# Kernel tuning notes

Measured on AMD Instinct MI355X. Metric: run time of the kernel, lower is better.

Reference implementation:

```python
import jax, jax.numpy as jnp
import numpy as np

ALPHA = 20.0 / 100.0  # dt / tau
ONE_MINUS_ALPHA = 1.0 - ALPHA


def setup_inputs() -> dict:
    key = jax.random.key(0)
    ks = jax.random.split(key, 7)
    T, B, I, H, O = 512, 256, 256, 1024, 128
    si, sh, so = 1.0 / np.sqrt(I), 1.0 / np.sqrt(H), 1.0 / np.sqrt(H)
    return {
        "x": jax.random.normal(ks[0], (T, B, I), dtype=jnp.float32),
        "Wi": jax.random.normal(ks[1], (H, I), dtype=jnp.float32) * si,
        "bi": jax.random.normal(ks[2], (H,), dtype=jnp.float32) * si,
        "Wh": jax.random.normal(ks[3], (H, H), dtype=jnp.float32) * sh,
        "bh": jax.random.normal(ks[4], (H,), dtype=jnp.float32) * sh,
        "Wo": jax.random.normal(ks[5], (O, H), dtype=jnp.float32) * so,
        "bo": jax.random.normal(ks[6], (O,), dtype=jnp.float32) * so,
    }


def reference(x, Wi, bi, Wh, bh, Wo, bo):
    T, B, I = x.shape
    H = Wh.shape[0]
    # Precompute input projection for all timesteps: [T, B, H]
    inp_proj = jnp.einsum("tbi,hi->tbh", x, Wi) + bi

    def step(carry, u_t):
        state, out = carry
        total = u_t + out @ Wh.T + bh
        state = state * ONE_MINUS_ALPHA + total * ALPHA
        out = jax.nn.relu(state)
        return (state, out), out

    init = (jnp.zeros((B, H), x.dtype), jnp.zeros((B, H), x.dtype))
    (_, _), rnn_activity = jax.lax.scan(step, init, inp_proj)  # [T, B, H]
    out = jnp.einsum("tbh,oh->tbo", rnn_activity, Wo) + bo  # [T, B, O]
    return out, rnn_activity
```

## Files before the change

kernel.cpp:

```cpp
#include <hip/hip_runtime.h>

using f4_t  = __attribute__((ext_vector_type(4))) float;
using bf8_t = __attribute__((ext_vector_type(8))) short;
using u32x4 = __attribute__((ext_vector_type(4))) unsigned int;

#define T_DIM 512
#define B_DIM 256
#define I_DIM 256
#define H_DIM 1024
#define O_DIM 128

#define SWZ(row, byte) ((byte) ^ (((row) & 7) << 4))

#define SMASK 0x8000800080008000ull

__device__ __forceinline__ unsigned short f2bf(float f) {
  unsigned u = __builtin_bit_cast(unsigned, f);
  return (unsigned short)((u + 0x7FFFu + ((u >> 16) & 1u)) >> 16);
}

__device__ __forceinline__ unsigned long long pack4bf(f4_t v) {
  unsigned long long r;
  r  = (unsigned long long)f2bf(v[0]);
  r |= (unsigned long long)f2bf(v[1]) << 16;
  r |= (unsigned long long)f2bf(v[2]) << 32;
  r |= (unsigned long long)f2bf(v[3]) << 48;
  return r;
}

__global__ __launch_bounds__(256, 1) void k_init(
    const float* __restrict__ Wi, const float* __restrict__ Wh,
    const float* __restrict__ Wo, unsigned short* __restrict__ Wi_b,
    unsigned short* __restrict__ Wh_b, unsigned short* __restrict__ Wo_b,
    unsigned short* __restrict__ hbuf1, unsigned* __restrict__ done) {
  int idx = blockIdx.x * 256 + threadIdx.x;
  int stride = gridDim.x * 256;
  for (int i = idx; i < H_DIM * H_DIM; i += stride) Wh_b[i] = f2bf(Wh[i]);
  for (int i = idx; i < H_DIM * I_DIM; i += stride) Wi_b[i] = f2bf(Wi[i]);
  for (int i = idx; i < O_DIM * H_DIM; i += stride) Wo_b[i] = f2bf(Wo[i]);
  for (int i = idx; i < B_DIM * H_DIM; i += stride) hbuf1[i] = 0x8000;
  for (int i = idx; i < 256 * 32; i += stride) done[i] = 0;
}

__global__ __launch_bounds__(256, 2) void k_inproj(
    const float* __restrict__ x, const unsigned short* __restrict__ Wi_b,
    const float* __restrict__ bi, float* __restrict__ act) {
  __shared__ unsigned short As[128 * 128];
  __shared__ unsigned short Bs[128 * 128];
  int blk = blockIdx.x;
  int mb = (blk & 7) * 128 + (blk >> 6);
  int nb = (blk >> 3) & 7;
  int m0 = mb * 128, n0 = nb * 128;
  int tid = threadIdx.x;
  int lane = tid & 63, w = tid >> 6;
  int wm0 = (w & 1) * 64, wn0 = (w >> 1) * 64;
  int lrow = lane & 15, lk = (lane >> 4) * 8;
  f4_t acc[4][4];
#pragma unroll
  for (int a = 0; a < 4; ++a)
#pragma unroll
    for (int b = 0; b < 4; ++b) acc[a][b] = (f4_t){0.f, 0.f, 0.f, 0.f};

  for (int kb = 0; kb < 2; ++kb) {
    if (kb) __syncthreads();
#pragma unroll
    for (int it = 0; it < 16; ++it) {
      int c = it * 256 + tid;
      int row = c >> 5;
      int kc = (c & 31) * 4;
      f4_t v = *(const f4_t*)(x + (size_t)(m0 + row) * I_DIM + kb * 128 + kc);
      *(unsigned long long*)((char*)As + SWZ(row, row * 256 + kc * 2)) = pack4bf(v);
    }
#pragma unroll
    for (int it = 0; it < 8; ++it) {
      int c = it * 256 + tid;
      int row = c >> 4;
      int k16 = c & 15;
      u32x4 v = *(const u32x4*)(Wi_b + (size_t)(n0 + row) * I_DIM + kb * 128 + k16 * 8);
      *(u32x4*)((char*)Bs + SWZ(row, row * 256 + k16 * 16)) = v;
    }
    __syncthreads();
#pragma unroll
    for (int ks = 0; ks < 4; ++ks) {
      bf8_t aF[4], bF[4];
#pragma unroll
      for (int mt = 0; mt < 4; ++mt) {
        int row = wm0 + mt * 16 + lrow;
        aF[mt] = *(const bf8_t*)((char*)As + SWZ(row, row * 256 + (ks * 32 + lk) * 2));
      }
#pragma unroll
      for (int nt = 0; nt < 4; ++nt) {
        int row = wn0 + nt * 16 + lrow;
        bF[nt] = *(const bf8_t*)((char*)Bs + SWZ(row, row * 256 + (ks * 32 + lk) * 2));
      }
#pragma unroll
      for (int mt = 0; mt < 4; ++mt)
#pragma unroll
        for (int nt = 0; nt < 4; ++nt)
          acc[mt][nt] =
              __builtin_amdgcn_mfma_f32_16x16x32_bf16(aF[mt], bF[nt], acc[mt][nt], 0, 0, 0);
    }
  }
#pragma unroll
  for (int nt = 0; nt < 4; ++nt) {
    int col = n0 + wn0 + nt * 16 + lrow;
    float bv = bi[col];
#pragma unroll
    for (int mt = 0; mt < 4; ++mt) {
      int rbase = m0 + wm0 + mt * 16 + (lane >> 4) * 4;
#pragma unroll
      for (int r = 0; r < 4; ++r)
        act[(size_t)(rbase + r) * H_DIM + col] = acc[mt][nt][r] + bv;
    }
  }
}

__global__ __launch_bounds__(256, 1) void k_scan(
    const unsigned short* __restrict__ Wh_b, const float* __restrict__ bh,
    float* __restrict__ act, unsigned short* __restrict__ hbuf0,
    unsigned short* __restrict__ hbuf1, unsigned* __restrict__ done) {
  __shared__ __align__(16) char hT[16 * 2048];
  __shared__ __align__(16) float pbuf[4][16][68];
  int blk = blockIdx.x;
  int g = blk & 15, hs = blk >> 4;
  int b0 = g * 16, h0 = hs * 64;
  int tid = threadIdx.x;
  int lane = tid & 63, w = tid >> 6;
  int lrow = lane & 15, lgq = lane >> 4, lk = lgq * 8;

  bf8_t Bf[4][8];
#pragma unroll
  for (int n = 0; n < 4; ++n)
#pragma unroll
    for (int kc = 0; kc < 8; ++kc)
      Bf[n][kc] = *(const bf8_t*)(Wh_b + (size_t)(h0 + n * 16 + lrow) * H_DIM +
                                  w * 256 + kc * 32 + lk);

  int pr = tid >> 4, pc = (tid & 15) * 4;
  float st[4] = {0.f, 0.f, 0.f, 0.f};
  f4_t bh4 = *(const f4_t*)(bh + h0 + pc);

  unsigned short* hb[2] = {hbuf0, hbuf1};
  unsigned* myslot = done + (g * 16 + hs) * 32;
  const unsigned* pollp = done + (g * 16 + (lane & 15)) * 32;
  bool dopoll = (lane < 16) && (lane != hs);

  int rh = tid >> 7;
  int colb = (tid & 127) * 16;

  f4_t ucur = *(const f4_t*)(act + (size_t)(b0 + pr) * H_DIM + h0 + pc);

  for (int t = 0; t < T_DIM; ++t) {
    int p = t & 1;
    const unsigned short* hprev = hb[p ^ 1];
    unsigned wtag = ((unsigned)(t - 1) >> 1) & 1u;
    unsigned want32 = wtag ? 0x80008000u : 0u;

    if (t > 0 && dopoll) {
      int gd = 0;
      while (__hip_atomic_load(pollp, __ATOMIC_RELAXED, __HIP_MEMORY_SCOPE_AGENT) <
                 (unsigned)t &&
             ++gd < 60000)
        __builtin_amdgcn_s_sleep(1);
    }
    __builtin_amdgcn_sched_barrier(0);

    const char* base = (const char*)(hprev + (size_t)b0 * H_DIM);
    unsigned long long a0 = (unsigned long long)(base + tid * 16);
    u32x4 q0, q1, q2, q3, q4, q5, q6, q7;
    asm volatile(
        "global_load_dwordx4 %[d0], %[a0], off sc0 sc1\n\t"
        "global_load_dwordx4 %[d1], %[a1], off sc0 sc1\n\t"
        "global_load_dwordx4 %[d2], %[a2], off sc0 sc1\n\t"
        "global_load_dwordx4 %[d3], %[a3], off sc0 sc1\n\t"
        "global_load_dwordx4 %[d4], %[a4], off sc0 sc1\n\t"
        "global_load_dwordx4 %[d5], %[a5], off sc0 sc1\n\t"
        "global_load_dwordx4 %[d6], %[a6], off sc0 sc1\n\t"
        "global_load_dwordx4 %[d7], %[a7], off sc0 sc1\n\t"
        "s_waitcnt vmcnt(0)"
        : [d0] "=&v"(q0), [d1] "=&v"(q1), [d2] "=&v"(q2), [d3] "=&v"(q3),
          [d4] "=&v"(q4), [d5] "=&v"(q5), [d6] "=&v"(q6), [d7] "=&v"(q7)
        : [a0] "v"(a0), [a1] "v"(a0 + 4096), [a2] "v"(a0 + 8192),
          [a3] "v"(a0 + 12288), [a4] "v"(a0 + 16384), [a5] "v"(a0 + 20480),
          [a6] "v"(a0 + 24576), [a7] "v"(a0 + 28672)
        : "memory");
    __builtin_amdgcn_sched_barrier(0);

    int tn = (t + 1 < T_DIM) ? t + 1 : t;
    f4_t unext = *(const f4_t*)(act + ((size_t)tn * B_DIM + b0 + pr) * H_DIM + h0 + pc);

#define STALE(qq) \
  ((((qq[0] ^ want32) | (qq[1] ^ want32) | (qq[2] ^ want32) | (qq[3] ^ want32)) & \
    0x80008000u) != 0u)
#define RELOAD(qq, ad)                                                          \
  asm volatile("global_load_dwordx4 %0, %1, off sc0 sc1\n\ts_waitcnt vmcnt(0)"  \
               : "=&v"(qq)                                                      \
               : "v"(ad)                                                        \
               : "memory")
    {
      int vg = 0;
      for (;;) {
        unsigned m = (STALE(q0) ? 1u : 0u) | (STALE(q1) ? 2u : 0u) |
                     (STALE(q2) ? 4u : 0u) | (STALE(q3) ? 8u : 0u) |
                     (STALE(q4) ? 16u : 0u) | (STALE(q5) ? 32u : 0u) |
                     (STALE(q6) ? 64u : 0u) | (STALE(q7) ? 128u : 0u);
        if (m == 0u || ++vg >= 400) break;
        __builtin_amdgcn_s_sleep(1);
        if (m & 1u) RELOAD(q0, a0);
        if (m & 2u) RELOAD(q1, a0 + 4096);
        if (m & 4u) RELOAD(q2, a0 + 8192);
        if (m & 8u) RELOAD(q3, a0 + 12288);
        if (m & 16u) RELOAD(q4, a0 + 16384);
        if (m & 32u) RELOAD(q5, a0 + 20480);
        if (m & 64u) RELOAD(q6, a0 + 24576);
        if (m & 128u) RELOAD(q7, a0 + 28672);
      }
    }
#undef STALE
#undef RELOAD
#pragma unroll
    for (int d = 0; d < 4; ++d) {
      q0[d] &= 0x7fff7fffu; q1[d] &= 0x7fff7fffu; q2[d] &= 0x7fff7fffu;
      q3[d] &= 0x7fff7fffu; q4[d] &= 0x7fff7fffu; q5[d] &= 0x7fff7fffu;
      q6[d] &= 0x7fff7fffu; q7[d] &= 0x7fff7fffu;
    }

#define STAGE(qq, r)                                                            \
  *(u32x4*)(&hT[(2 * (r) + rh) * 2048 + SWZ(2 * (r) + rh, colb)]) = qq
    STAGE(q0, 0); STAGE(q1, 1); STAGE(q2, 2); STAGE(q3, 3);
    STAGE(q4, 4); STAGE(q5, 5); STAGE(q6, 6); STAGE(q7, 7);
#undef STAGE
    asm volatile("s_waitcnt lgkmcnt(0)\ns_barrier" ::: "memory");
    __builtin_amdgcn_sched_barrier(0);

    f4_t acc[4];
#pragma unroll
    for (int n = 0; n < 4; ++n) acc[n] = (f4_t){0.f, 0.f, 0.f, 0.f};
#pragma unroll
    for (int kc = 0; kc < 8; ++kc) {
      int cbyte = w * 512 + kc * 64 + lgq * 16;
      bf8_t Af = *(const bf8_t*)(&hT[lrow * 2048 + SWZ(lrow, cbyte)]);
#pragma unroll
      for (int n = 0; n < 4; ++n)
        acc[n] = __builtin_amdgcn_mfma_f32_16x16x32_bf16(Af, Bf[n][kc], acc[n], 0, 0, 0);
    }

#pragma unroll
    for (int n = 0; n < 4; ++n)
#pragma unroll
      for (int r = 0; r < 4; ++r)
        pbuf[w][lgq * 4 + r][n * 16 + lrow] = acc[n][r];
    asm volatile("s_waitcnt lgkmcnt(0)\ns_barrier" ::: "memory");
    __builtin_amdgcn_sched_barrier(0);

    f4_t s0 = *(const f4_t*)&pbuf[0][pr][pc];
    f4_t s1 = *(const f4_t*)&pbuf[1][pr][pc];
    f4_t s2 = *(const f4_t*)&pbuf[2][pr][pc];
    f4_t s3 = *(const f4_t*)&pbuf[3][pr][pc];
    f4_t tot = s0 + s1 + s2 + s3 + ucur + bh4;
    f4_t hres;
#pragma unroll
    for (int j = 0; j < 4; ++j) {
      st[j] = st[j] * 0.8f + tot[j] * 0.2f;
      hres[j] = fmaxf(st[j], 0.f);
    }

    unsigned long long hp = pack4bf(hres) | (((t >> 1) & 1) ? SMASK : 0ull);
    __hip_atomic_store(
        (unsigned long long*)(hb[p] + (size_t)(b0 + pr) * H_DIM + h0 + pc), hp,
        __ATOMIC_RELAXED, __HIP_MEMORY_SCOPE_AGENT);

    asm volatile("s_barrier" ::: "memory");
    if (tid == 0)
      __hip_atomic_store(myslot, (unsigned)(t + 1), __ATOMIC_RELAXED,
                         __HIP_MEMORY_SCOPE_AGENT);

    *(f4_t*)(act + ((size_t)t * B_DIM + b0 + pr) * H_DIM + h0 + pc) = hres;
    ucur = unext;
  }
}

__global__ __launch_bounds__(256, 2) void k_outproj(
    const float* __restrict__ act, const unsigned short* __restrict__ Wo_b,
    const float* __restrict__ bo, float* __restrict__ out) {
  __shared__ unsigned short As[128 * 64];
  __shared__ unsigned short Bs[128 * 64];
  int m0 = blockIdx.x * 128;
  int tid = threadIdx.x;
  int lane = tid & 63, w = tid >> 6;
  int wm0 = (w & 1) * 64, wn0 = (w >> 1) * 64;
  int lrow = lane & 15, lk = (lane >> 4) * 8;
  f4_t acc[4][4];
#pragma unroll
  for (int a = 0; a < 4; ++a)
#pragma unroll
    for (int b = 0; b < 4; ++b) acc[a][b] = (f4_t){0.f, 0.f, 0.f, 0.f};

  for (int kb = 0; kb < 16; ++kb) {
    if (kb) __syncthreads();
#pragma unroll
    for (int it = 0; it < 8; ++it) {
      int c = it * 256 + tid;
      int row = c >> 4;
      int kc = (c & 15) * 4;
      f4_t v = *(const f4_t*)(act + (size_t)(m0 + row) * H_DIM + kb * 64 + kc);
      *(unsigned long long*)((char*)As + SWZ(row, row * 128 + kc * 2)) = pack4bf(v);
    }
#pragma unroll
    for (int it = 0; it < 4; ++it) {
      int c = it * 256 + tid;
      int row = c >> 3;
      int k16 = c & 7;
      u32x4 v = *(const u32x4*)(Wo_b + (size_t)row * H_DIM + kb * 64 + k16 * 8);
      *(u32x4*)((char*)Bs + SWZ(row, row * 128 + k16 * 16)) = v;
    }
    __syncthreads();
#pragma unroll
    for (int ks = 0; ks < 2; ++ks) {
      bf8_t aF[4], bF[4];
#pragma unroll
      for (int mt = 0; mt < 4; ++mt) {
        int row = wm0 + mt * 16 + lrow;
        aF[mt] = *(const bf8_t*)((char*)As + SWZ(row, row * 128 + (ks * 32 + lk) * 2));
      }
#pragma unroll
      for (int nt = 0; nt < 4; ++nt) {
        int row = wn0 + nt * 16 + lrow;
        bF[nt] = *(const bf8_t*)((char*)Bs + SWZ(row, row * 128 + (ks * 32 + lk) * 2));
      }
#pragma unroll
      for (int mt = 0; mt < 4; ++mt)
#pragma unroll
        for (int nt = 0; nt < 4; ++nt)
          acc[mt][nt] =
              __builtin_amdgcn_mfma_f32_16x16x32_bf16(aF[mt], bF[nt], acc[mt][nt], 0, 0, 0);
    }
  }
#pragma unroll
  for (int nt = 0; nt < 4; ++nt) {
    int col = wn0 + nt * 16 + lrow;
    float bv = bo[col];
#pragma unroll
    for (int mt = 0; mt < 4; ++mt) {
      int rbase = m0 + wm0 + mt * 16 + (lane >> 4) * 4;
#pragma unroll
      for (int r = 0; r < 4; ++r)
        out[(size_t)(rbase + r) * O_DIM + col] = acc[mt][nt][r] + bv;
    }
  }
}

extern "C" void kernel_launch(void* const* d_in, const int* in_sizes, int n_in,
                              void* d_out, int out_size, void* d_ws, size_t ws_size,
                              hipStream_t stream) {
  const float* x  = (const float*)d_in[0];
  const float* Wi = (const float*)d_in[1];
  const float* bi = (const float*)d_in[2];
  const float* Wh = (const float*)d_in[3];
  const float* bh = (const float*)d_in[4];
  const float* Wo = (const float*)d_in[5];
  const float* bo = (const float*)d_in[6];

  float* out = (float*)d_out;
  float* act = out + (size_t)T_DIM * B_DIM * O_DIM;

  char* ws = (char*)d_ws;
  unsigned short* Wh_b  = (unsigned short*)(ws);
  unsigned short* Wi_b  = (unsigned short*)(ws + (2u << 20));
  unsigned short* Wo_b  = (unsigned short*)(ws + (2u << 20) + (512u << 10));
  unsigned short* hbuf0 = (unsigned short*)(ws + (2u << 20) + (768u << 10));
  unsigned short* hbuf1 = (unsigned short*)(ws + (2u << 20) + (1280u << 10));
  unsigned* done        = (unsigned*)(ws + (2u << 20) + (1792u << 10));

  k_init<<<1024, 256, 0, stream>>>(Wi, Wh, Wo, Wi_b, Wh_b, Wo_b, hbuf1, done);
  k_inproj<<<8192, 256, 0, stream>>>(x, Wi_b, bi, act);
  k_scan<<<256, 256, 0, stream>>>(Wh_b, bh, act, hbuf0, hbuf1, done);
  k_outproj<<<1024, 256, 0, stream>>>(act, Wo_b, bo, out);
}
```

Before: 1.612 ms.

## Halve scan workgroups to 128 with 512 threads each covering 128 hidden columns

The recurrent scan kernel now uses 128 workgroups of 512 threads, each owning a 16-batch by 128-hidden tile instead of 16 by 64. Each batch group has 8 participants instead of 16, so the per-step cross-workgroup polling and flag traffic shrink, and every block loads the previous hidden state half as often overall. Waves are arranged as two column halves by four K slices. The LDS swizzle is widened to 16 rows, and the hidden-state store becomes an inline-asm global store with sc0 sc1 bits. The cost is more work per block on each serial step and half as many CUs in use.

New measurement: 1.618 ms. No clear change (+0.4%).

```diff
diff --git a/kernel.cpp b/kernel.cpp
--- a/kernel.cpp
+++ b/kernel.cpp
@@ -11,6 +11,7 @@
 #define O_DIM 128
 
 #define SWZ(row, byte) ((byte) ^ (((row) & 7) << 4))
+#define HSWZ(row, byte) ((byte) ^ (((row) & 15) << 4))
 
 #define SMASK 0x8000800080008000ull
 
@@ -115,46 +116,44 @@
   }
 }
 
-__global__ __launch_bounds__(256, 1) void k_scan(
+__global__ __launch_bounds__(512, 1) void k_scan(
     const unsigned short* __restrict__ Wh_b, const float* __restrict__ bh,
     float* __restrict__ act, unsigned short* __restrict__ hbuf0,
     unsigned short* __restrict__ hbuf1, unsigned* __restrict__ done) {
   __shared__ __align__(16) char hT[16 * 2048];
-  __shared__ __align__(16) float pbuf[4][16][68];
+  __shared__ __align__(16) float pbuf[4][16][132];
   int blk = blockIdx.x;
   int g = blk & 15, hs = blk >> 4;
-  int b0 = g * 16, h0 = hs * 64;
+  int b0 = g * 16, h0 = hs * 128;
   int tid = threadIdx.x;
   int lane = tid & 63, w = tid >> 6;
-  int lrow = lane & 15, lgq = lane >> 4, lk = lgq * 8;
+  int nb = w & 1, ks = w >> 1;
+  int lrow = lane & 15, lgq = lane >> 4;
 
   bf8_t Bf[4][8];
 #pragma unroll
   for (int n = 0; n < 4; ++n)
 #pragma unroll
     for (int kc = 0; kc < 8; ++kc)
-      Bf[n][kc] = *(const bf8_t*)(Wh_b + (size_t)(h0 + n * 16 + lrow) * H_DIM +
-                                  w * 256 + kc * 32 + lk);
-
-  int pr = tid >> 4, pc = (tid & 15) * 4;
+      Bf[n][kc] = *(const bf8_t*)(Wh_b +
+                                  (size_t)(h0 + nb * 64 + n * 16 + lrow) * H_DIM +
+                                  ks * 256 + kc * 32 + lgq * 8);
+
+  int pr = tid >> 5, pc = (tid & 31) * 4;
   float st[4] = {0.f, 0.f, 0.f, 0.f};
   f4_t bh4 = *(const f4_t*)(bh + h0 + pc);
 
   unsigned short* hb[2] = {hbuf0, hbuf1};
-  unsigned* myslot = done + (g * 16 + hs) * 32;
-  const unsigned* pollp = done + (g * 16 + (lane & 15)) * 32;
-  bool dopoll = (lane < 16) && (lane != hs);
-
-  int rh = tid >> 7;
-  int colb = (tid & 127) * 16;
+  unsigned* myslot = done + (g * 8 + hs) * 32;
+  const unsigned* pollp = done + (g * 8 + (lane & 7)) * 32;
+  bool dopoll = (lane < 8) && (lane != hs);
 
   f4_t ucur = *(const f4_t*)(act + (size_t)(b0 + pr) * H_DIM + h0 + pc);
 
   for (int t = 0; t < T_DIM; ++t) {
     int p = t & 1;
     const unsigned short* hprev = hb[p ^ 1];
-    unsigned wtag = ((unsigned)(t - 1) >> 1) & 1u;
-    unsigned want32 = wtag ? 0x80008000u : 0u;
+    unsigned want32 = ((((unsigned)(t - 1) >> 1) & 1u) ? 0x80008000u : 0u);
 
     if (t > 0 && dopoll) {
       int gd = 0;
@@ -167,22 +166,16 @@
 
     const char* base = (const char*)(hprev + (size_t)b0 * H_DIM);
     unsigned long long a0 = (unsigned long long)(base + tid * 16);
-    u32x4 q0, q1, q2, q3, q4, q5, q6, q7;
+    u32x4 q0, q1, q2, q3;
     asm volatile(
         "global_load_dwordx4 %[d0], %[a0], off sc0 sc1\n\t"
         "global_load_dwordx4 %[d1], %[a1], off sc0 sc1\n\t"
         "global_load_dwordx4 %[d2], %[a2], off sc0 sc1\n\t"
         "global_load_dwordx4 %[d3], %[a3], off sc0 sc1\n\t"
-        "global_load_dwordx4 %[d4], %[a4], off sc0 sc1\n\t"
-        "global_load_dwordx4 %[d5], %[a5], off sc0 sc1\n\t"
-        "global_load_dwordx4 %[d6], %[a6], off sc0 sc1\n\t"
-        "global_load_dwordx4 %[d7], %[a7], off sc0 sc1\n\t"
         "s_waitcnt vmcnt(0)"
-        : [d0] "=&v"(q0), [d1] "=&v"(q1), [d2] "=&v"(q2), [d3] "=&v"(q3),
-          [d4] "=&v"(q4), [d5] "=&v"(q5), [d6] "=&v"(q6), [d7] "=&v"(q7)
-        : [a0] "v"(a0), [a1] "v"(a0 + 4096), [a2] "v"(a0 + 8192),
-          [a3] "v"(a0 + 12288), [a4] "v"(a0 + 16384), [a5] "v"(a0 + 20480),
-          [a6] "v"(a0 + 24576), [a7] "v"(a0 + 28672)
+        : [d0] "=&v"(q0), [d1] "=&v"(q1), [d2] "=&v"(q2), [d3] "=&v"(q3)
+        : [a0] "v"(a0), [a1] "v"(a0 + 8192), [a2] "v"(a0 + 16384),
+          [a3] "v"(a0 + 24576)
         : "memory");
     __builtin_amdgcn_sched_barrier(0);
 
@@ -201,34 +194,28 @@
       int vg = 0;
       for (;;) {
         unsigned m = (STALE(q0) ? 1u : 0u) | (STALE(q1) ? 2u : 0u) |
-                     (STALE(q2) ? 4u : 0u) | (STALE(q3) ? 8u : 0u) |
-                     (STALE(q4) ? 16u : 0u) | (STALE(q5) ? 32u : 0u) |
-                     (STALE(q6) ? 64u : 0u) | (STALE(q7) ? 128u : 0u);
+                     (STALE(q2) ? 4u : 0u) | (STALE(q3) ? 8u : 0u);
         if (m == 0u || ++vg >= 400) break;
         __builtin_amdgcn_s_sleep(1);
         if (m & 1u) RELOAD(q0, a0);
-        if (m & 2u) RELOAD(q1, a0 + 4096);
-        if (m & 4u) RELOAD(q2, a0 + 8192);
-        if (m & 8u) RELOAD(q3, a0 + 12288);
-        if (m & 16u) RELOAD(q4, a0 + 16384);
-        if (m & 32u) RELOAD(q5, a0 + 20480);
-        if (m & 64u) RELOAD(q6, a0 + 24576);
-        if (m & 128u) RELOAD(q7, a0 + 28672);
+        if (m & 2u) RELOAD(q1, a0 + 8192);
+        if (m & 4u) RELOAD(q2, a0 + 16384);
+        if (m & 8u) RELOAD(q3, a0 + 24576);
       }
     }
 #undef STALE
 #undef RELOAD
 #pragma unroll
     for (int d = 0; d < 4; ++d) {
-      q0[d] &= 0x7fff7fffu; q1[d] &= 0x7fff7fffu; q2[d] &= 0x7fff7fffu;
-      q3[d] &= 0x7fff7fffu; q4[d] &= 0x7fff7fffu; q5[d] &= 0x7fff7fffu;
-      q6[d] &= 0x7fff7fffu; q7[d] &= 0x7fff7fffu;
-    }
-
-#define STAGE(qq, r)                                                            \
-  *(u32x4*)(&hT[(2 * (r) + rh) * 2048 + SWZ(2 * (r) + rh, colb)]) = qq
+      q0[d] &= 0x7fff7fffu; q1[d] &= 0x7fff7fffu;
+      q2[d] &= 0x7fff7fffu; q3[d] &= 0x7fff7fffu;
+    }
+
+    int rh = tid >> 7;
+    int colb = (tid & 127) * 16;
+#define STAGE(qq, k)                                                            \
+  *(u32x4*)(&hT[((k) * 4 + rh) * 2048 + HSWZ((k) * 4 + rh, colb)]) = qq
     STAGE(q0, 0); STAGE(q1, 1); STAGE(q2, 2); STAGE(q3, 3);
-    STAGE(q4, 4); STAGE(q5, 5); STAGE(q6, 6); STAGE(q7, 7);
 #undef STAGE
     asm volatile("s_waitcnt lgkmcnt(0)\ns_barrier" ::: "memory");
     __builtin_amdgcn_sched_barrier(0);
@@ -238,8 +225,8 @@
     for (int n = 0; n < 4; ++n) acc[n] = (f4_t){0.f, 0.f, 0.f, 0.f};
 #pragma unroll
     for (int kc = 0; kc < 8; ++kc) {
-      int cbyte = w * 512 + kc * 64 + lgq * 16;
-      bf8_t Af = *(const bf8_t*)(&hT[lrow * 2048 + SWZ(lrow, cbyte)]);
+      int cbyte = ks * 512 + kc * 64 + lgq * 16;
+      bf8_t Af = *(const bf8_t*)(&hT[lrow * 2048 + HSWZ(lrow, cbyte)]);
 #pragma unroll
       for (int n = 0; n < 4; ++n)
         acc[n] = __builtin_amdgcn_mfma_f32_16x16x32_bf16(Af, Bf[n][kc], acc[n], 0, 0, 0);
@@ -249,7 +236,7 @@
     for (int n = 0; n < 4; ++n)
 #pragma unroll
       for (int r = 0; r < 4; ++r)
-        pbuf[w][lgq * 4 + r][n * 16 + lrow] = acc[n][r];
+        pbuf[ks][lgq * 4 + r][nb * 64 + n * 16 + lrow] = acc[n][r];
     asm volatile("s_waitcnt lgkmcnt(0)\ns_barrier" ::: "memory");
     __builtin_amdgcn_sched_barrier(0);
 
@@ -266,9 +253,10 @@
     }
 
     unsigned long long hp = pack4bf(hres) | (((t >> 1) & 1) ? SMASK : 0ull);
-    __hip_atomic_store(
-        (unsigned long long*)(hb[p] + (size_t)(b0 + pr) * H_DIM + h0 + pc), hp,
-        __ATOMIC_RELAXED, __HIP_MEMORY_SCOPE_AGENT);
+    unsigned long long sa =
+        (unsigned long long)(hb[p] + (size_t)(b0 + pr) * H_DIM + h0 + pc);
+    asm volatile("global_store_dwordx2 %0, %1, off sc0 sc1" ::"v"(sa), "v"(hp)
+                 : "memory");
 
     asm volatile("s_barrier" ::: "memory");
     if (tid == 0)
@@ -374,6 +362,6 @@
 
   k_init<<<1024, 256, 0, stream>>>(Wi, Wh, Wo, Wi_b, Wh_b, Wo_b, hbuf1, done);
   k_inproj<<<8192, 256, 0, stream>>>(x, Wi_b, bi, act);
-  k_scan<<<256, 256, 0, stream>>>(Wh_b, bh, act, hbuf0, hbuf1, done);
+  k_scan<<<128, 512, 0, stream>>>(Wh_b, bh, act, hbuf0, hbuf1, done);
   k_outproj<<<1024, 256, 0, stream>>>(act, Wo_b, bo, out);
 }
```
